# Kernel tuning notes

Measured on AMD Instinct MI355X. Metric: run time of the kernel, lower is better.

Reference implementation:

```python
import jax, jax.numpy as jnp
import numpy as np

GRID_SIZE = 5
NUM_BASES = 2 ** GRID_SIZE - 1  # 31: actual number of Haar bases produced by the loop

def _haar_edges():
    left, mid, right = [], [], []
    for level in range(GRID_SIZE):
        scale = 2 ** level
        for shift in range(scale):
            left.append(shift / scale)
            mid.append((shift + 0.5) / scale)
            right.append((shift + 1.0) / scale)
    return (np.asarray(left, np.float32), np.asarray(mid, np.float32), np.asarray(right, np.float32))

_LEFT, _MID, _RIGHT = _haar_edges()


def setup_inputs() -> dict:
    key = jax.random.key(0)
    k1, k2, k3 = jax.random.split(key, 3)
    B, IN, OUT = 16384, 256, 256
    x = jax.random.normal(k1, (B, IN), dtype=jnp.float32)
    base_weight = jax.random.normal(k2, (OUT, IN), dtype=jnp.float32) * 0.05
    spline_weight = jax.random.normal(k3, (OUT, IN, NUM_BASES), dtype=jnp.float32) * 0.05
    spline_scaler = jnp.ones((OUT, IN), dtype=jnp.float32)
    return {"x": x, "base_weight": base_weight, "spline_weight": spline_weight, "spline_scaler": spline_scaler}


def reference(x, base_weight, spline_weight, spline_scaler):
    # per-feature min/max normalization over the batch dim
    x_min = jnp.min(x, axis=0, keepdims=True)
    x_max = jnp.max(x, axis=0, keepdims=True)
    xn = (x - x_min) / (x_max - x_min + 1e-8)            # [B, IN]
    left = jnp.asarray(_LEFT, x.dtype)
    mid = jnp.asarray(_MID, x.dtype)
    right = jnp.asarray(_RIGHT, x.dtype)
    xe = xn[..., None]                                    # [B, IN, 1]
    mask1 = ((xe >= left) & (xe < mid)).astype(x.dtype)
    mask2 = ((xe >= mid) & (xe < right)).astype(x.dtype)
    bases = mask1 - mask2                                 # [B, IN, NB]
    base_out = jax.nn.relu(x) @ base_weight.T             # [B, OUT]
    sw = spline_weight * spline_scaler[..., None]         # [OUT, IN, NB]
    wavelet_out = jnp.einsum('bik,oik->bo', bases, sw)    # [B, OUT]
    return base_out + wavelet_out
```

## Files before the change

### kernel.cpp

```cpp
#include <hip/hip_runtime.h>
#include <stdint.h>

typedef short s16x8 __attribute__((ext_vector_type(8)));
typedef float f32x4 __attribute__((ext_vector_type(4)));

#define IN_F   256
#define OUT_F  256
#define BATCH  16384
#define NB     31
#define KONE   8192
#define KTOT   8448

typedef const __attribute__((address_space(1))) void* as1cvp;
typedef __attribute__((address_space(3))) void* as3vp;

__device__ __forceinline__ unsigned short f2bf(float f) {
    unsigned u = __float_as_uint(f);
    u += 0x7FFFu + ((u >> 16) & 1u);
    return (unsigned short)(u >> 16);
}

__global__ __launch_bounds__(256) void prep1(
    const float* __restrict__ x, const float* __restrict__ bw,
    const float* __restrict__ sw, const float* __restrict__ sc,
    float* __restrict__ pmn, float* __restrict__ pmx,
    unsigned short* __restrict__ Wb) {
    const int blk = blockIdx.x, t = threadIdx.x;
    if (blk < 256) {
        const int b0 = blk * 64;
        float mn = 3.4e38f, mx = -3.4e38f;
        for (int r = 0; r < 64; ++r) {
            float v = x[(size_t)(b0 + r) * IN_F + t];
            mn = fminf(mn, v);
            mx = fmaxf(mx, v);
        }
        pmn[blk * 256 + t] = mn;
        pmx[blk * 256 + t] = mx;
    } else {
        const int o = blk - 256, i = t;
        const float s = sc[o * IN_F + i];
        const float* swp = sw + (size_t)(o * IN_F + i) * NB;
        float w[NB];
#pragma unroll
        for (int k = 0; k < NB; ++k) w[k] = swp[k];
        unsigned short* dst = Wb + (size_t)o * KTOT + i * 32;
#pragma unroll
        for (int q = 0; q < 4; ++q) {
            union { s16x8 v; unsigned short s8[8]; } pk;
#pragma unroll
            for (int e = 0; e < 8; ++e) {
                int j = q * 8 + e;
                float acc = 0.f;
#pragma unroll
                for (int l = 0; l < 5; ++l) {
                    int kk = (1 << l) - 1 + (j >> (5 - l));
                    acc += (((j >> (4 - l)) & 1) ? -w[kk] : w[kk]);
                }
                pk.s8[e] = f2bf(acc * s);
            }
            *(s16x8*)(dst + q * 8) = pk.v;
        }
        Wb[(size_t)o * KTOT + KONE + i] = f2bf(bw[o * IN_F + i]);
    }
}

__global__ __launch_bounds__(256) void leaf2t(
    const float* __restrict__ x, const float* __restrict__ pmn,
    const float* __restrict__ pmx, unsigned char* __restrict__ lt) {
    __shared__ unsigned char lsh[256 * 68];
    __shared__ float xminsh[IN_F], rdnsh[IN_F];
    const int t = threadIdx.x;
    {
        float mn0 = 3.4e38f, mn1 = 3.4e38f, mx0 = -3.4e38f, mx1 = -3.4e38f;
#pragma unroll 8
        for (int b = 0; b < 256; b += 2) {
            mn0 = fminf(mn0, pmn[(size_t)b * 256 + t]);
            mn1 = fminf(mn1, pmn[(size_t)(b + 1) * 256 + t]);
            mx0 = fmaxf(mx0, pmx[(size_t)b * 256 + t]);
            mx1 = fmaxf(mx1, pmx[(size_t)(b + 1) * 256 + t]);
        }
        float mn = fminf(mn0, mn1), mx = fmaxf(mx0, mx1);
        xminsh[t] = mn;
        rdnsh[t] = 1.0f / (mx - mn + 1e-8f);
    }
    __syncthreads();
    const float xmn = xminsh[t], rdn = rdnsh[t];
    const int b0 = blockIdx.x * 64;
    for (int r = 0; r < 64; ++r) {
        float v = x[(size_t)(b0 + r) * IN_F + t];
        float xn = (v - xmn) * rdn;
        int l = (int)(xn * 32.0f);
        lsh[t * 68 + r] = (l >= 0 && l < 32) ? (unsigned char)l : (unsigned char)255;
    }
    __syncthreads();
    const int lane = t & 63, w = t >> 6;
    const unsigned* lshU = (const unsigned*)lsh;
#pragma unroll
    for (int ib = 0; ib < 16; ++ib) {
        int i = ib * 16 + w * 4 + (lane >> 4);
        unsigned val = lshU[i * 17 + (lane & 15)];
        *(unsigned*)(lt + (size_t)i * BATCH + b0 + (lane & 15) * 4) = val;
    }
}

__global__ __launch_bounds__(128, 2) void gemm_kan(
    const float* __restrict__ x,
    const unsigned short* __restrict__ Wb,
    const unsigned char* __restrict__ lt,
    float* __restrict__ out)
{
    __shared__ unsigned short Ash[64 * 64];
    __shared__ unsigned short Bsh[4 * 64 * 64];

    const int t     = threadIdx.x;
    const int lane  = t & 63;
    const int wv    = t >> 6;
    const int mtile = blockIdx.x;
    const int ntile = blockIdx.y;

    {
        uint4 z; z.x = z.y = z.z = z.w = 0u;
        uint4* a4 = (uint4*)(Ash + wv * 2048);
#pragma unroll
        for (int r = 0; r < 4; ++r) a4[lane + r * 64] = z;
    }

    const unsigned char* bbase = (const unsigned char*)(Wb
        + (size_t)(ntile * 64 + wv * 32 + (lane >> 3)) * KTOT
        + (((lane & 7) ^ (lane >> 3)) << 3));

    const int am = t >> 1;
    const int ag = t & 1;
    const size_t lrow0 = (size_t)mtile * 64;
    int ps = -1;

    const int rr = lane & 15, kq = lane >> 4;
    f32x4 acc[2][4] = {};

#define STAGE(KB, SLOT)                                                        \
    {                                                                          \
        const unsigned char* _s = bbase + (size_t)(KB) * 128;                  \
        unsigned short* _d = Bsh + (SLOT) * 4096 + wv * 2048;                  \
        _Pragma("unroll")                                                      \
        for (int q = 0; q < 4; ++q)                                            \
            __builtin_amdgcn_global_load_lds(                                  \
                (as1cvp)(_s + (size_t)q * 8 * KTOT * 2),                       \
                (as3vp)(uint32_t)(uintptr_t)(_d + q * 512), 16, 0, 0);         \
    }

#define AONEHOT(LF)                                                            \
    {                                                                          \
        if (ps >= 0) Ash[ps] = 0;                                              \
        int l = (LF);                                                          \
        if (l < 32) {                                                          \
            int c = (ag << 2) + (l >> 3);                                      \
            ps = (am << 6) + ((c ^ (am & 7)) << 3) + (l & 7);                  \
            Ash[ps] = 0x3F80;                                                  \
        } else ps = -1;                                                        \
    }

#define BARRIER()                                                              \
    asm volatile("" ::: "memory");                                             \
    __builtin_amdgcn_s_barrier();                                              \
    asm volatile("" ::: "memory")

#define MFMAPH(KB)                                                             \
    {                                                                          \
        const unsigned short* bb = Bsh + ((KB) & 3) * 4096;                    \
        __builtin_amdgcn_s_setprio(1);                                         \
        _Pragma("unroll")                                                      \
        for (int ks = 0; ks < 2; ++ks) {                                       \
            const int c = (ks << 2) + kq;                                      \
            s16x8 af[2], bfr[4];                                               \
            _Pragma("unroll")                                                  \
            for (int mt = 0; mt < 2; ++mt) {                                   \
                int m = wv * 32 + mt * 16 + rr;                                \
                af[mt] = *(const s16x8*)&Ash[(m << 6) + ((c ^ (m & 7)) << 3)]; \
            }                                                                  \
            _Pragma("unroll")                                                  \
            for (int nt = 0; nt < 4; ++nt) {                                   \
                int n = nt * 16 + rr;                                          \
                bfr[nt] = *(const s16x8*)&bb[(n << 6) + ((c ^ (n & 7)) << 3)]; \
            }                                                                  \
            _Pragma("unroll")                                                  \
            for (int mt = 0; mt < 2; ++mt)                                     \
                _Pragma("unroll")                                              \
                for (int nt = 0; nt < 4; ++nt)                                 \
                    acc[mt][nt] = __builtin_amdgcn_mfma_f32_16x16x32_bf16(     \
                        af[mt], bfr[nt], acc[mt][nt], 0, 0, 0);                \
        }                                                                      \
        __builtin_amdgcn_s_setprio(0);                                         \
    }

    STAGE(0, 0);
    unsigned char lf0 = lt[(size_t)(0 + ag) * BATCH + lrow0 + am];
    STAGE(1, 1);
    unsigned char lf1 = lt[(size_t)(2 + ag) * BATCH + lrow0 + am];

    for (int kb = 0; kb < 126; kb += 2) {
        asm volatile("s_waitcnt vmcnt(5)" ::: "memory");
        AONEHOT(lf0);
        STAGE(kb + 2, (kb + 2) & 3);
        lf0 = lt[(size_t)((kb + 2) * 2 + ag) * BATCH + lrow0 + am];
        BARRIER();
        MFMAPH(kb);
        asm volatile("s_waitcnt vmcnt(5)" ::: "memory");
        AONEHOT(lf1);
        STAGE(kb + 3, (kb + 3) & 3);
        lf1 = lt[(size_t)((kb + 3) * 2 + ag) * BATCH + lrow0 + am];
        BARRIER();
        MFMAPH(kb + 1);
    }

    asm volatile("s_waitcnt vmcnt(5)" ::: "memory");
    AONEHOT(lf0);
    STAGE(128, 0);
    BARRIER();
    MFMAPH(126);

    asm volatile("s_waitcnt vmcnt(4)" ::: "memory");
    AONEHOT(lf1);
    STAGE(129, 1);
    BARRIER();
    MFMAPH(127);

#pragma unroll
    for (int kb = 128; kb < 132; ++kb) {
        if (kb < 131) { asm volatile("s_waitcnt vmcnt(4)" ::: "memory"); }
        else          { asm volatile("s_waitcnt vmcnt(0)" ::: "memory"); }
        {
            const float* xr = x + (size_t)(mtile * 64 + wv * 32) * IN_F + (kb - 128) * 64 + lane;
            const int cslot = (lane >> 3);
#pragma unroll
            for (int m0 = 0; m0 < 32; ++m0) {
                int m = wv * 32 + m0;
                float v = xr[(size_t)m0 * IN_F];
                Ash[(m << 6) + ((cslot ^ (m & 7)) << 3) + (lane & 7)] = f2bf(fmaxf(v, 0.0f));
            }
        }
        if (kb + 2 < 132) STAGE(kb + 2, (kb + 2) & 3);
        BARRIER();
        MFMAPH(kb);
    }

    const int rq = lane >> 4;
#pragma unroll
    for (int mt = 0; mt < 2; ++mt)
#pragma unroll
        for (int nt = 0; nt < 4; ++nt)
#pragma unroll
            for (int v = 0; v < 4; ++v) {
                int row = mtile * 64 + wv * 32 + mt * 16 + rq * 4 + v;
                int col = ntile * 64 + nt * 16 + rr;
                out[(size_t)row * OUT_F + col] = acc[mt][nt][v];
            }
#undef STAGE
#undef AONEHOT
#undef BARRIER
#undef MFMAPH
}

extern "C" void kernel_launch(void* const* d_in, const int* in_sizes, int n_in,
                              void* d_out, int out_size, void* d_ws, size_t ws_size,
                              hipStream_t stream) {
    (void)in_sizes; (void)n_in; (void)out_size; (void)ws_size;
    const float* x  = (const float*)d_in[0];
    const float* bw = (const float*)d_in[1];
    const float* sw = (const float*)d_in[2];
    const float* sc = (const float*)d_in[3];
    float* out = (float*)d_out;

    char* ws = (char*)d_ws;
    unsigned short* Wb = (unsigned short*)ws;
    unsigned char*  lt = (unsigned char*)(ws + 4325376);
    float* pmn = (float*)(ws + 8519680);
    float* pmx = (float*)(ws + 8781824);

    prep1<<<512, 256, 0, stream>>>(x, bw, sw, sc, pmn, pmx, Wb);
    leaf2t<<<256, 256, 0, stream>>>(x, pmn, pmx, lt);
    gemm_kan<<<dim3(256, 4), 128, 0, stream>>>(x, Wb, lt, out);
}
```

Baseline: 162.4 us.

## Use 128x128 GEMM tiles with two-way split-K and atomic accumulation

Moves the KAN GEMM from 64x64 tiles with 2 waves to 128x128 tiles with 4 waves per block. This doubles operand reuse per LDS load, and the B staging goes to a 3-slot rotating buffer. To keep enough blocks in flight, K is split into two halves via blockIdx.z, and results are combined with float atomicAdd into an output that prep1 now zeroes. The cost is atomic traffic, an extra zeroing pass, nondeterministic summation order and more barriers per step.

Result: slower. 165.8 us (+2.0%).

```diff
diff --git a/kernel.cpp b/kernel.cpp
--- a/kernel.cpp
+++ b/kernel.cpp
@@ -24,7 +24,7 @@
     const float* __restrict__ x, const float* __restrict__ bw,
     const float* __restrict__ sw, const float* __restrict__ sc,
     float* __restrict__ pmn, float* __restrict__ pmx,
-    unsigned short* __restrict__ Wb) {
+    unsigned short* __restrict__ Wb, float* __restrict__ outz) {
     const int blk = blockIdx.x, t = threadIdx.x;
     if (blk < 256) {
         const int b0 = blk * 64;
@@ -36,7 +36,7 @@
         }
         pmn[blk * 256 + t] = mn;
         pmx[blk * 256 + t] = mx;
-    } else {
+    } else if (blk < 512) {
         const int o = blk - 256, i = t;
         const float s = sc[o * IN_F + i];
         const float* swp = sw + (size_t)(o * IN_F + i) * NB;
@@ -61,6 +61,11 @@
             *(s16x8*)(dst + q * 8) = pk.v;
         }
         Wb[(size_t)o * KTOT + KONE + i] = f2bf(bw[o * IN_F + i]);
+    } else {
+        float4 z; z.x = z.y = z.z = z.w = 0.f;
+        float4* oz = (float4*)outz + (size_t)(blk - 512) * 4096;
+#pragma unroll
+        for (int r = 0; r < 16; ++r) oz[t + r * 256] = z;
     }
 }
 
@@ -103,44 +108,52 @@
     }
 }
 
-__global__ __launch_bounds__(128, 2) void gemm_kan(
+__global__ __launch_bounds__(256, 2) void gemm_kan(
     const float* __restrict__ x,
     const unsigned short* __restrict__ Wb,
     const unsigned char* __restrict__ lt,
     float* __restrict__ out)
 {
-    __shared__ unsigned short Ash[64 * 64];
-    __shared__ unsigned short Bsh[4 * 64 * 64];
+    __shared__ unsigned short Ash[128 * 64];
+    __shared__ unsigned short Bsh[3 * 128 * 64];
 
     const int t     = threadIdx.x;
     const int lane  = t & 63;
     const int wv    = t >> 6;
+    const int wm    = wv >> 1, wn = wv & 1;
     const int mtile = blockIdx.x;
     const int ntile = blockIdx.y;
+    const int zz    = blockIdx.z;
+    const int kbeg  = zz ? 66 : 0;
+    const int kend1 = zz ? 128 : 66;
+
+    const int rr = lane & 15, kq = lane >> 4;
+    const int mbase = mtile * 128;
 
     {
         uint4 z; z.x = z.y = z.z = z.w = 0u;
-        uint4* a4 = (uint4*)(Ash + wv * 2048);
-#pragma unroll
-        for (int r = 0; r < 4; ++r) a4[lane + r * 64] = z;
-    }
+        uint4* a4 = (uint4*)Ash;
+#pragma unroll
+        for (int r = 0; r < 4; ++r) a4[t + r * 256] = z;
+    }
+    asm volatile("s_waitcnt lgkmcnt(0)" ::: "memory");
 
     const unsigned char* bbase = (const unsigned char*)(Wb
-        + (size_t)(ntile * 64 + wv * 32 + (lane >> 3)) * KTOT
+        + (size_t)(ntile * 128 + wv * 32 + (lane >> 3)) * KTOT
         + (((lane & 7) ^ (lane >> 3)) << 3));
 
     const int am = t >> 1;
     const int ag = t & 1;
-    const size_t lrow0 = (size_t)mtile * 64;
     int ps = -1;
 
-    const int rr = lane & 15, kq = lane >> 4;
-    f32x4 acc[2][4] = {};
+    f32x4 acc[4][4] = {};
+
+#define FENCE() asm volatile("" ::: "memory")
 
 #define STAGE(KB, SLOT)                                                        \
     {                                                                          \
         const unsigned char* _s = bbase + (size_t)(KB) * 128;                  \
-        unsigned short* _d = Bsh + (SLOT) * 4096 + wv * 2048;                  \
+        unsigned short* _d = Bsh + (SLOT) * 8192 + wv * 2048;                  \
         _Pragma("unroll")                                                      \
         for (int q = 0; q < 4; ++q)                                            \
             __builtin_amdgcn_global_load_lds(                                  \
@@ -159,31 +172,30 @@
         } else ps = -1;                                                        \
     }
 
-#define BARRIER()                                                              \
-    asm volatile("" ::: "memory");                                             \
-    __builtin_amdgcn_s_barrier();                                              \
-    asm volatile("" ::: "memory")
-
-#define MFMAPH(KB)                                                             \
+#define BAR_A()  FENCE(); __builtin_amdgcn_s_barrier(); FENCE()
+#define BAR_B()  asm volatile("s_waitcnt lgkmcnt(0)" ::: "memory");            \
+                 __builtin_amdgcn_s_barrier(); FENCE()
+
+#define MFMAPH(SLOT)                                                           \
     {                                                                          \
-        const unsigned short* bb = Bsh + ((KB) & 3) * 4096;                    \
+        const unsigned short* bb = Bsh + (SLOT) * 8192;                        \
         __builtin_amdgcn_s_setprio(1);                                         \
         _Pragma("unroll")                                                      \
         for (int ks = 0; ks < 2; ++ks) {                                       \
             const int c = (ks << 2) + kq;                                      \
-            s16x8 af[2], bfr[4];                                               \
+            s16x8 af[4], bfr[4];                                               \
             _Pragma("unroll")                                                  \
-            for (int mt = 0; mt < 2; ++mt) {                                   \
-                int m = wv * 32 + mt * 16 + rr;                                \
+            for (int mt = 0; mt < 4; ++mt) {                                   \
+                int m = wm * 64 + mt * 16 + rr;                                \
                 af[mt] = *(const s16x8*)&Ash[(m << 6) + ((c ^ (m & 7)) << 3)]; \
             }                                                                  \
             _Pragma("unroll")                                                  \
             for (int nt = 0; nt < 4; ++nt) {                                   \
-                int n = nt * 16 + rr;                                          \
+                int n = wn * 64 + nt * 16 + rr;                                \
                 bfr[nt] = *(const s16x8*)&bb[(n << 6) + ((c ^ (n & 7)) << 3)]; \
             }                                                                  \
             _Pragma("unroll")                                                  \
-            for (int mt = 0; mt < 2; ++mt)                                     \
+            for (int mt = 0; mt < 4; ++mt)                                     \
                 _Pragma("unroll")                                              \
                 for (int nt = 0; nt < 4; ++nt)                                 \
                     acc[mt][nt] = __builtin_amdgcn_mfma_f32_16x16x32_bf16(     \
@@ -192,72 +204,121 @@
         __builtin_amdgcn_s_setprio(0);                                         \
     }
 
-    STAGE(0, 0);
-    unsigned char lf0 = lt[(size_t)(0 + ag) * BATCH + lrow0 + am];
-    STAGE(1, 1);
-    unsigned char lf1 = lt[(size_t)(2 + ag) * BATCH + lrow0 + am];
-
-    for (int kb = 0; kb < 126; kb += 2) {
+    STAGE(kbeg, 0);
+    FENCE();
+    unsigned char lfa = lt[(size_t)(kbeg * 2 + ag) * BATCH + mbase + am];
+    FENCE();
+    STAGE(kbeg + 1, 1);
+    FENCE();
+    unsigned char lfb = lt[(size_t)((kbeg + 1) * 2 + ag) * BATCH + mbase + am];
+    FENCE();
+
+    int sA = 0, sB = 1, sC = 2;
+
+    for (int kb = kbeg; kb < kend1 - 2; kb += 2) {
+        BAR_A();
         asm volatile("s_waitcnt vmcnt(5)" ::: "memory");
-        AONEHOT(lf0);
-        STAGE(kb + 2, (kb + 2) & 3);
-        lf0 = lt[(size_t)((kb + 2) * 2 + ag) * BATCH + lrow0 + am];
-        BARRIER();
-        MFMAPH(kb);
+        AONEHOT(lfa);
+        FENCE();
+        STAGE(kb + 2, sC);
+        FENCE();
+        lfa = lt[(size_t)((kb + 2) * 2 + ag) * BATCH + mbase + am];
+        FENCE();
+        BAR_B();
+        MFMAPH(sA);
+        BAR_A();
         asm volatile("s_waitcnt vmcnt(5)" ::: "memory");
-        AONEHOT(lf1);
-        STAGE(kb + 3, (kb + 3) & 3);
-        lf1 = lt[(size_t)((kb + 3) * 2 + ag) * BATCH + lrow0 + am];
-        BARRIER();
-        MFMAPH(kb + 1);
-    }
-
+        AONEHOT(lfb);
+        FENCE();
+        STAGE(kb + 3, sA);
+        FENCE();
+        lfb = lt[(size_t)((kb + 3) * 2 + ag) * BATCH + mbase + am];
+        FENCE();
+        BAR_B();
+        MFMAPH(sB);
+        int tmp = sC; sC = sB; sB = sA; sA = tmp;
+    }
+
+    BAR_A();
     asm volatile("s_waitcnt vmcnt(5)" ::: "memory");
-    AONEHOT(lf0);
-    STAGE(128, 0);
-    BARRIER();
-    MFMAPH(126);
-
-    asm volatile("s_waitcnt vmcnt(4)" ::: "memory");
-    AONEHOT(lf1);
-    STAGE(129, 1);
-    BARRIER();
-    MFMAPH(127);
-
-#pragma unroll
-    for (int kb = 128; kb < 132; ++kb) {
-        if (kb < 131) { asm volatile("s_waitcnt vmcnt(4)" ::: "memory"); }
-        else          { asm volatile("s_waitcnt vmcnt(0)" ::: "memory"); }
-        {
-            const float* xr = x + (size_t)(mtile * 64 + wv * 32) * IN_F + (kb - 128) * 64 + lane;
-            const int cslot = (lane >> 3);
-#pragma unroll
-            for (int m0 = 0; m0 < 32; ++m0) {
-                int m = wv * 32 + m0;
-                float v = xr[(size_t)m0 * IN_F];
-                Ash[(m << 6) + ((cslot ^ (m & 7)) << 3) + (lane & 7)] = f2bf(fmaxf(v, 0.0f));
-            }
+    AONEHOT(lfa);
+    FENCE();
+    if (zz) { STAGE(kend1, sC); FENCE(); }
+    BAR_B();
+    MFMAPH(sA);
+
+    BAR_A();
+    if (zz) { asm volatile("s_waitcnt vmcnt(4)" ::: "memory"); }
+    else    { asm volatile("s_waitcnt vmcnt(0)" ::: "memory"); }
+    AONEHOT(lfb);
+    FENCE();
+    if (zz) { STAGE(kend1 + 1, sA); FENCE(); }
+    BAR_B();
+    MFMAPH(sB);
+
+    if (zz) {
+#define DENSEA(KB)                                                             \
+        {                                                                      \
+            const float* xr = x + (size_t)(mbase + wv * 32) * IN_F             \
+                                + ((KB) - 128) * 64 + lane;                    \
+            const int cslot = (lane >> 3);                                     \
+            _Pragma("unroll")                                                  \
+            for (int m0 = 0; m0 < 32; ++m0) {                                  \
+                int m = wv * 32 + m0;                                          \
+                float v = xr[(size_t)m0 * IN_F];                               \
+                Ash[(m << 6) + ((cslot ^ (m & 7)) << 3) + (lane & 7)] =        \
+                    f2bf(fmaxf(v, 0.0f));                                      \
+            }                                                                  \
         }
-        if (kb + 2 < 132) STAGE(kb + 2, (kb + 2) & 3);
-        BARRIER();
-        MFMAPH(kb);
+        BAR_A();
+        asm volatile("s_waitcnt vmcnt(4)" ::: "memory");
+        DENSEA(128);
+        FENCE();
+        STAGE(130, sB);
+        FENCE();
+        BAR_B();
+        MFMAPH(sC);
+
+        BAR_A();
+        asm volatile("s_waitcnt vmcnt(4)" ::: "memory");
+        DENSEA(129);
+        FENCE();
+        STAGE(131, sC);
+        FENCE();
+        BAR_B();
+        MFMAPH(sA);
+
+        BAR_A();
+        asm volatile("s_waitcnt vmcnt(4)" ::: "memory");
+        DENSEA(130);
+        BAR_B();
+        MFMAPH(sB);
+
+        BAR_A();
+        asm volatile("s_waitcnt vmcnt(0)" ::: "memory");
+        DENSEA(131);
+        BAR_B();
+        MFMAPH(sC);
+#undef DENSEA
     }
 
     const int rq = lane >> 4;
 #pragma unroll
-    for (int mt = 0; mt < 2; ++mt)
+    for (int mt = 0; mt < 4; ++mt)
 #pragma unroll
         for (int nt = 0; nt < 4; ++nt)
 #pragma unroll
             for (int v = 0; v < 4; ++v) {
-                int row = mtile * 64 + wv * 32 + mt * 16 + rq * 4 + v;
-                int col = ntile * 64 + nt * 16 + rr;
-                out[(size_t)row * OUT_F + col] = acc[mt][nt][v];
+                int row = mbase + wm * 64 + mt * 16 + rq * 4 + v;
+                int col = ntile * 128 + wn * 64 + nt * 16 + rr;
+                atomicAdd(&out[(size_t)row * OUT_F + col], acc[mt][nt][v]);
             }
 #undef STAGE
 #undef AONEHOT
-#undef BARRIER
+#undef BAR_A
+#undef BAR_B
 #undef MFMAPH
+#undef FENCE
 }
 
 extern "C" void kernel_launch(void* const* d_in, const int* in_sizes, int n_in,
@@ -276,7 +337,7 @@
     float* pmn = (float*)(ws + 8519680);
     float* pmx = (float*)(ws + 8781824);
 
-    prep1<<<512, 256, 0, stream>>>(x, bw, sw, sc, pmn, pmx, Wb);
+    prep1<<<768, 256, 0, stream>>>(x, bw, sw, sc, pmn, pmx, Wb, out);
     leaf2t<<<256, 256, 0, stream>>>(x, pmn, pmx, lt);
-    gemm_kan<<<dim3(256, 4), 128, 0, stream>>>(x, Wb, lt, out);
-}
+    gemm_kan<<<dim3(128, 2, 2), 256, 0, stream>>>(x, Wb, lt, out);
+}
```
